# Performance work log

Hardware: AMD Instinct MI355X
Metric: run time of the kernel (lower is better)

The kernel has to match this reference:

```python
import jax, jax.numpy as jnp
import numpy as np

N = 100000   # nodes per node type ('net' and 'cell')
E = 600000   # edges per canonical relation
D_IN = 16    # raw input feature dim
D = 128      # hidden dim (in_size == out_size, required by wl: Linear(2*D -> D))
SLOPE = 0.2  # DGL GATConv leaky_relu negative slope


def setup_inputs() -> dict:
    key = jax.random.key(0)
    ks = jax.random.split(key, 24)
    f = lambda k, shp, scale=1.0: jax.random.normal(k, shp, dtype=jnp.float32) * scale
    s_in = 1.0 / np.sqrt(D_IN).astype(np.float32)
    s_d = 1.0 / np.sqrt(D).astype(np.float32)
    s_2d = 1.0 / np.sqrt(2 * D).astype(np.float32)
    inp = {
        'x_net':   f(ks[0], (N, D_IN)),
        'x_cell':  f(ks[1], (N, D_IN)),
        'Wp_net':  f(ks[2], (D, D_IN), s_in),
        'Wp_cell': f(ks[3], (D, D_IN), s_in),
        # per-edge-type GATConv params: fc weight + attn_l + attn_r (num_heads=1, no bias)
        'Wg0': f(ks[4], (D, D), s_d), 'al0': f(ks[5], (D,), s_d), 'ar0': f(ks[6], (D,), s_d),
        'Wg1': f(ks[7], (D, D), s_d), 'al1': f(ks[8], (D,), s_d), 'ar1': f(ks[9], (D,), s_d),
        'Wg2': f(ks[10], (D, D), s_d), 'al2': f(ks[11], (D,), s_d), 'ar2': f(ks[12], (D,), s_d),
        'Wl':   f(ks[13], (D, 2 * D), s_2d),
        'bias': jnp.zeros((D,), jnp.float32),
        # edge lists: relation 0 = cell->net, 1 = net->cell, 2 = net->net
        'src0': jax.random.randint(ks[14], (E,), 0, N, dtype=jnp.int32),
        'dst0': jax.random.randint(ks[15], (E,), 0, N, dtype=jnp.int32),
        'src1': jax.random.randint(ks[16], (E,), 0, N, dtype=jnp.int32),
        'dst1': jax.random.randint(ks[17], (E,), 0, N, dtype=jnp.int32),
        'src2': jax.random.randint(ks[18], (E,), 0, N, dtype=jnp.int32),
        'dst2': jax.random.randint(ks[19], (E,), 0, N, dtype=jnp.int32),
    }
    return inp


def _gat(x_src, x_dst, W, al, ar, src, dst):
    """DGL GATConv (num_heads=1, bias=False) on one relation's edge list."""
    h_src = x_src @ W.T                               # [N, D]
    h_dst = x_dst @ W.T                               # [N, D]
    el = (h_src @ al)[src]                            # [E] gathered src logits
    er = (h_dst @ ar)[dst]                            # [E] gathered dst logits
    e = jax.nn.leaky_relu(el + er, SLOPE)             # [E]
    # segment softmax over incoming edges of each dst node
    m = jax.ops.segment_max(e, dst, num_segments=N)
    ex = jnp.exp(e - m[dst])
    denom = jax.ops.segment_sum(ex, dst, num_segments=N)
    alpha = ex / denom[dst]                           # [E]
    return jax.ops.segment_sum(h_src[src] * alpha[:, None], dst, num_segments=N)


def reference(x_net, x_cell, Wp_net, Wp_cell,
              Wg0, al0, ar0, Wg1, al1, ar1, Wg2, al2, ar2,
              Wl, bias,
              src0, dst0, src1, dst1, src2, dst2):
    # feature projection per node type (ParaGraph.feat_proj)
    h_net = x_net @ Wp_net.T                          # [N, D]
    h_cell = x_cell @ Wp_cell.T                       # [N, D]
    feat = {'net': h_net, 'cell': h_cell}
    out = {'net': jnp.zeros((N, D), h_net.dtype), 'cell': jnp.zeros((N, D), h_cell.dtype)}
    # canonical etypes: (srctype, dsttype, gat params, edge list)
    rels = [
        ('cell', 'net', Wg0, al0, ar0, src0, dst0),
        ('net', 'cell', Wg1, al1, ar1, src1, dst1),
        ('net', 'net',  Wg2, al2, ar2, src2, dst2),
    ]
    for st, dt, W, al, ar, src, dst in rels:
        out[dt] = out[dt] + _gat(feat[st], feat[dt], W, al, ar, src, dst)
        # faithful to the original: concat+linear+relu recomputed for EVERY ntype
        # inside the etype loop (the redundant fused-op pattern)
        for nt in ('net', 'cell'):
            out[nt] = jax.nn.relu(
                jnp.concatenate([feat[nt], out[nt] + bias], axis=1) @ Wl.T)
    return jnp.stack([out['net'], out['cell']])      # [2, N, D]
```

## Files before the change

### kernel.cpp

```cpp
#include <hip/hip_runtime.h>
#include <hip/hip_bf16.h>
#include <stdint.h>

#define NN 100000
#define NE 600000
#define SP 136
#define NB 782
#define BCAP 1600
#define CHUNK 4096
#define NCH 147
#define GB 1563
#define AB 6250

typedef unsigned short u16;
typedef unsigned int u32;
typedef __attribute__((ext_vector_type(8))) short short8;
typedef __attribute__((ext_vector_type(8))) __bf16 bf16x8;
typedef __attribute__((ext_vector_type(4))) float floatx4;

__device__ __forceinline__ float b2f(u16 u) {
  union { float f; u32 i; } c; c.i = ((u32)u) << 16; return c.f;
}
__device__ __forceinline__ u16 f2b(float f) {
  union { float f; u32 i; } c; c.f = f;
  u32 r = c.i + 0x7FFFu + ((c.i >> 16) & 1u);
  return (u16)(r >> 16);
}


__device__ __forceinline__ void gemm_w(const u16* __restrict__ W, int ldw, u16* __restrict__ C,
                                       u16* lds, int tid, int row0, const bf16x8* a,
                                       int m16, int quad, int wv) {
#pragma unroll
  for (int it = 0; it < 8; ++it) {
    int idx = it * 256 + tid;
    int r = idx >> 4, c = (idx & 15) << 3;
    *(short8*)(&lds[r * SP + c]) = *(const short8*)(W + (size_t)r * ldw + c);
  }
  __syncthreads();
  const u16* brow = &lds[m16 * SP + quad * 8];
  floatx4 acc[8];
#pragma unroll
  for (int c = 0; c < 8; ++c) acc[c] = floatx4{0.f, 0.f, 0.f, 0.f};
#pragma unroll
  for (int kk = 0; kk < 4; ++kk) {
#pragma unroll
    for (int c = 0; c < 8; ++c) {
      bf16x8 bfr = *(const bf16x8*)(brow + c * 16 * SP + kk * 32);
      acc[c] = __builtin_amdgcn_mfma_f32_16x16x32_bf16(a[kk], bfr, acc[c], 0, 0, 0);
    }
  }
#pragma unroll
  for (int c = 0; c < 8; ++c) {
    int col = c * 16 + m16;
#pragma unroll
    for (int r = 0; r < 4; ++r) {
      int grow = row0 + wv * 16 + quad * 4 + r;
      if (grow < NN) C[(size_t)grow * 128 + col] = f2b(acc[c][r]);
    }
  }
}

template<int FINAL>
__device__ __forceinline__ void fused_body(int blk, int tid, const u16* __restrict__ A,
                                           const u16* __restrict__ P, void* __restrict__ C,
                                           const u16* __restrict__ W, const float* __restrict__ cvec,
                                           u16* Wlds) {
  const int row0 = blk * 64;
#pragma unroll
  for (int it = 0; it < 8; ++it) {
    int idx = it * 256 + tid;
    int r = idx >> 4, c = (idx & 15) << 3;
    *(short8*)(&Wlds[r * SP + c]) = *(const short8*)(W + (size_t)r * 256 + c);
  }
  const int lane = tid & 63, wv = tid >> 6;
  const int m16 = lane & 15, quad = lane >> 4;
  int arow = row0 + wv * 16 + m16;
  if (arow >= NN) arow = NN - 1;
  const u16* Ab = A + (size_t)arow * 128 + quad * 8;
  bf16x8 a[4];
#pragma unroll
  for (int kk = 0; kk < 4; ++kk) a[kk] = *(const bf16x8*)(Ab + kk * 32);
  __syncthreads();
  const u16* brow = &Wlds[m16 * SP + quad * 8];
  floatx4 acc[8];
#pragma unroll
  for (int c = 0; c < 8; ++c) acc[c] = floatx4{0.f, 0.f, 0.f, 0.f};
#pragma unroll
  for (int kk = 0; kk < 4; ++kk) {
#pragma unroll
    for (int c = 0; c < 8; ++c) {
      bf16x8 bfr = *(const bf16x8*)(brow + c * 16 * SP + kk * 32);
      acc[c] = __builtin_amdgcn_mfma_f32_16x16x32_bf16(a[kk], bfr, acc[c], 0, 0, 0);
    }
  }
#pragma unroll
  for (int c = 0; c < 8; ++c) {
    int col = c * 16 + m16;
    float cv = cvec[col];
#pragma unroll
    for (int r = 0; r < 4; ++r) {
      int grow = row0 + wv * 16 + quad * 4 + r;
      if (grow < NN) {
        float v = acc[c][r] + b2f(P[(size_t)grow * 128 + col]) + cv;
        v = fmaxf(v, 0.f);
        if (FINAL) ((float*)C)[(size_t)grow * 128 + col] = v;
        else       ((u16*)C)[(size_t)grow * 128 + col] = f2b(v);
      }
    }
  }
}

template<int RMW>
__device__ __forceinline__ void agg_body(int nb, int tid, const u16* __restrict__ h,
                                         const u32* __restrict__ srecs, const int* __restrict__ rp,
                                         const float* __restrict__ el, const float* __restrict__ er,
                                         u16* __restrict__ out) {
  int sub = tid & 15;
  int n = nb * 16 + (tid >> 4);
  int start = rp[n], end = rp[n + 1];
  u16* orow = out + (size_t)n * 128 + sub * 8;
  if (start == end) {
    if (!RMW) *(short8*)orow = short8{0, 0, 0, 0, 0, 0, 0, 0};
    return;
  }
  float ern = er[n];
  float acc[8];
#pragma unroll
  for (int t = 0; t < 8; ++t) acc[t] = 0.f;
  float sl = 0.f;
  const u16* hsub = h + sub * 8;
  for (int base = start; base < end; base += 16) {
    int m = end - base; if (m > 16) m = 16;
    int srci = 0; float w = 0.f;
    if (sub < m) {
      srci = (int)srecs[base + sub];
      float l = el[srci] + ern;
      l = (l >= 0.f) ? l : 0.2f * l;
      w = __expf(l);
    }
    sl += w;
    for (int i = 0; i < m; ++i) {
      float x = __shfl(w, i, 16);
      int sv = __shfl(srci, i, 16);
      short8 hv = *(const short8*)(hsub + (size_t)sv * 128);
#pragma unroll
      for (int t = 0; t < 8; ++t) acc[t] += x * b2f((u16)hv[t]);
    }
  }
  float s = sl;
#pragma unroll
  for (int off = 8; off > 0; off >>= 1) s += __shfl_xor(s, off, 16);
  float inv = 1.f / s;
  short8 o;
  if (RMW) {
    short8 pv = *(const short8*)orow;
#pragma unroll
    for (int t = 0; t < 8; ++t) o[t] = (short)f2b(b2f((u16)pv[t]) + acc[t] * inv);
  } else {
#pragma unroll
    for (int t = 0; t < 8; ++t) o[t] = (short)f2b(acc[t] * inv);
  }
  *(short8*)orow = o;
}


__global__ __launch_bounds__(256) void prep_k(const float* __restrict__ x_net, const float* __restrict__ x_cell,
                                              const float* __restrict__ Wp_net, const float* __restrict__ Wp_cell,
                                              u16* __restrict__ feat_net, u16* __restrict__ feat_cell,
                                              const float* __restrict__ Wl, const float* __restrict__ Wg0,
                                              const float* __restrict__ Wg1, const float* __restrict__ Wg2,
                                              u16* __restrict__ Wl_bf, u16* __restrict__ Wg_bf,
                                              const float* al0, const float* ar0, const float* al1,
                                              const float* ar1, const float* al2, const float* ar2,
                                              const float* bias, float* __restrict__ vecs,
                                              int* __restrict__ bcnt) {
  int bid = blockIdx.x, tid = threadIdx.x;
  if (bid < 2 * AB) {
    int y = bid >= AB;
    int bx = y ? bid - AB : bid;
    const float* x  = y ? x_cell : x_net;
    const float* Wp = y ? Wp_cell : Wp_net;
    u16* feat       = y ? feat_cell : feat_net;
    __shared__ float Ws[128 * 17];
    __shared__ float xs[16][17];
#pragma unroll
    for (int it = 0; it < 8; ++it) {
      int idx = it * 256 + tid;
      int j = idx >> 4, k = idx & 15;
      Ws[j * 17 + k] = Wp[idx];
    }
    int n0 = bx * 16;
    { int nn = tid >> 4, k = tid & 15;
      xs[nn][k] = x[(size_t)(n0 + nn) * 16 + k]; }
    __syncthreads();
    int j = tid & 127, g = tid >> 7;
    float acc[8];
#pragma unroll
    for (int r = 0; r < 8; ++r) acc[r] = 0.f;
#pragma unroll
    for (int k = 0; k < 16; ++k) {
      float w = Ws[j * 17 + k];
#pragma unroll
      for (int r = 0; r < 8; ++r) acc[r] += xs[g * 8 + r][k] * w;
    }
#pragma unroll
    for (int r = 0; r < 8; ++r)
      feat[(size_t)(n0 + g * 8 + r) * 128 + j] = f2b(acc[r]);
  } else if (bid < 2 * AB + 128) {
    int cid = bid - 2 * AB;
    int y = cid >> 5, bx = cid & 31;
    const float* src = (y == 0) ? Wl : (y == 1) ? Wg0 : (y == 2) ? Wg1 : Wg2;
    u16* dst = (y == 0) ? Wl_bf : Wg_bf + (size_t)(y - 1) * 16384;
    int n = (y == 0) ? 32768 : 16384;
    int i = (bx * 256 + tid) * 4;
    if (i >= n) return;
    float4 v = *(const float4*)(src + i);
    ushort4 p; p.x = f2b(v.x); p.y = f2b(v.y); p.z = f2b(v.z); p.w = f2b(v.w);
    *(ushort4*)(dst + i) = p;
  } else if (bid < 2 * AB + 135) {
    int a = bid - (2 * AB + 128);
    if (tid >= 128) return;
    int j = tid;
    float s = 0.f;
    if (a < 6) {
      const float* W = (a < 2) ? Wg0 : (a < 4) ? Wg1 : Wg2;
      const float* v = (a == 0) ? al0 : (a == 1) ? ar0 : (a == 2) ? al1 : (a == 3) ? ar1 : (a == 4) ? al2 : ar2;
      for (int i = 0; i < 128; ++i) s += W[i * 128 + j] * v[i];
    } else {
      for (int i = 0; i < 128; ++i) s += Wl[(size_t)j * 256 + 128 + i] * bias[i];
    }
    vecs[a * 128 + j] = s;
  } else {
    int r = bid - (2 * AB + 135);
    for (int i = tid; i < NB; i += 256) bcnt[(size_t)r * NB + i] = 0;
  }
}

__global__ __launch_bounds__(256) void logbh_k(const u16* __restrict__ feat_net, const u16* __restrict__ feat_cell,
                                               const float* __restrict__ vecs, float* __restrict__ outs,
                                               const int* __restrict__ dst0, const int* __restrict__ dst1,
                                               const int* __restrict__ dst2, int* __restrict__ bcnt) {
  __shared__ int sm[NB];
  int bid = blockIdx.x, tid = threadIdx.x;
  if (bid < 782) {
    float* vs = (float*)sm;
#pragma unroll
    for (int it = 0; it < 3; ++it) vs[it * 256 + tid] = vecs[it * 256 + tid];
    __syncthreads();
    int y = bid >= 391;
    int bx = y ? bid - 391 : bid;
    const u16* f = y ? feat_cell : feat_net;
    int n = bx * 256 + tid;
    if (n >= NN) return;
    const u16* row = f + (size_t)n * 128;
    if (y == 0) {
      float s1 = 0.f, s2 = 0.f, s4 = 0.f, s5 = 0.f;
#pragma unroll
      for (int k = 0; k < 128; k += 8) {
        short8 u = *(const short8*)(row + k);
#pragma unroll
        for (int t = 0; t < 8; ++t) {
          float fv = b2f((u16)u[t]);
          s1 += fv * vs[1 * 128 + k + t]; s2 += fv * vs[2 * 128 + k + t];
          s4 += fv * vs[4 * 128 + k + t]; s5 += fv * vs[5 * 128 + k + t];
        }
      }
      outs[(size_t)1 * NN + n] = s1; outs[(size_t)2 * NN + n] = s2;
      outs[(size_t)4 * NN + n] = s4; outs[(size_t)5 * NN + n] = s5;
    } else {
      float s0 = 0.f, s3 = 0.f;
#pragma unroll
      for (int k = 0; k < 128; k += 8) {
        short8 u = *(const short8*)(row + k);
#pragma unroll
        for (int t = 0; t < 8; ++t) {
          float fv = b2f((u16)u[t]);
          s0 += fv * vs[0 * 128 + k + t]; s3 += fv * vs[3 * 128 + k + t];
        }
      }
      outs[(size_t)0 * NN + n] = s0; outs[(size_t)3 * NN + n] = s3;
    }
  } else {
    int e = bid - 782;
    int r = e / NCH, bx = e % NCH;
    const int* dst = (r == 0) ? dst0 : (r == 1) ? dst1 : dst2;
    for (int i = tid; i < NB; i += 256) sm[i] = 0;
    __syncthreads();
    int e0 = bx * CHUNK;
    int cnt = NE - e0; if (cnt > CHUNK) cnt = CHUNK;
    for (int i = tid; i < cnt; i += 256) atomicAdd(&sm[((u32)dst[e0 + i]) >> 7], 1);
    __syncthreads();
    for (int b = tid; b < NB; b += 256) {
      int c = sm[b];
      if (c) atomicAdd(&bcnt[(size_t)r * NB + b], c);
    }
  }
}

__global__ __launch_bounds__(1024) void bscan_k(const int* __restrict__ bcnt, int* __restrict__ bptr,
                                                int* __restrict__ bcur) {
  int r = blockIdx.x, t = threadIdx.x;
  const int* c = bcnt + (size_t)r * NB;
  int* p = bptr + (size_t)r * (NB + 1);
  int* cur = bcur + (size_t)r * NB;
  int v = (t < NB) ? c[t] : 0;
  __shared__ int ss[1024];
  ss[t] = v; __syncthreads();
  for (int off = 1; off < 1024; off <<= 1) {
    int u = (t >= off) ? ss[t - off] : 0;
    __syncthreads();
    ss[t] += u;
    __syncthreads();
  }
  if (t < NB) { int e = ss[t] - v; p[t] = e; cur[t] = e; }
  if (t == 1023) p[NB] = ss[1023];
}

__global__ __launch_bounds__(256) void bscatter_k(const int* __restrict__ src0, const int* __restrict__ dst0,
                                                  const int* __restrict__ src1, const int* __restrict__ dst1,
                                                  const int* __restrict__ src2, const int* __restrict__ dst2,
                                                  int* __restrict__ bcur, u32* __restrict__ recs) {
  int r = blockIdx.y;
  const int* src = (r == 0) ? src0 : (r == 1) ? src1 : src2;
  const int* dst = (r == 0) ? dst0 : (r == 1) ? dst1 : dst2;
  __shared__ int hist[NB];
  __shared__ int lstart[NB];
  __shared__ int lcur[NB];
  __shared__ int badj[NB];
  __shared__ u32 rbuf[CHUNK];
  __shared__ u16 kbuf[CHUNK];
  __shared__ int ss[256];
  int tid = threadIdx.x;
  int e0 = blockIdx.x * CHUNK;
  int cnt = NE - e0; if (cnt > CHUNK) cnt = CHUNK;

  for (int i = tid; i < NB; i += 256) hist[i] = 0;
  __syncthreads();
  for (int i = tid; i < cnt; i += 256) atomicAdd(&hist[((u32)dst[e0 + i]) >> 7], 1);
  __syncthreads();
  int loc[4]; int s = 0;
  int base4 = tid * 4;
#pragma unroll
  for (int j = 0; j < 4; ++j) {
    int idx = base4 + j;
    int v = (idx < NB) ? hist[idx] : 0;
    loc[j] = s; s += v;
  }
  ss[tid] = s; __syncthreads();
  for (int off = 1; off < 256; off <<= 1) {
    int u = (tid >= off) ? ss[tid - off] : 0;
    __syncthreads();
    ss[tid] += u;
    __syncthreads();
  }
  int ex = ss[tid] - s;
#pragma unroll
  for (int j = 0; j < 4; ++j) {
    int idx = base4 + j;
    if (idx < NB) { int e = ex + loc[j]; lstart[idx] = e; lcur[idx] = e; }
  }
  __syncthreads();
  for (int b = tid; b < NB; b += 256) {
    int c = hist[b];
    int g = 0;
    if (c) g = atomicAdd(&bcur[(size_t)r * NB + b], c);
    badj[b] = g - lstart[b];
  }
  __syncthreads();
  for (int i = tid; i < cnt; i += 256) {
    int dN = dst[e0 + i], sN = src[e0 + i];
    int b = ((u32)dN) >> 7;
    int pos = atomicAdd(&lcur[b], 1);
    rbuf[pos] = ((u32)(dN & 127) << 17) | (u32)sN;
    kbuf[pos] = (u16)b;
  }
  __syncthreads();
  u32* out = recs + (size_t)r * NE;
  for (int i = tid; i < cnt; i += 256) {
    int b = kbuf[i];
    out[badj[b] + i] = rbuf[i];
  }
}

__global__ __launch_bounds__(256) void sortgemm_k(u32* __restrict__ recs, const int* __restrict__ bptr,
                                                  int* __restrict__ rowptr,
                                                  const u16* __restrict__ feat_net, const u16* __restrict__ feat_cell,
                                                  const u16* __restrict__ Wl_bf, const u16* __restrict__ Wg_bf,
                                                  u16* __restrict__ P_net, u16* __restrict__ P_cell,
                                                  u16* __restrict__ h0, u16* __restrict__ h1, u16* __restrict__ h2) {
  __shared__ u32 smem[128 * SP / 2];
  int bid = blockIdx.x, tid = threadIdx.x;
  if (bid < 3 * NB) {
    int r = bid / NB, b = bid % NB;
    const int* p = bptr + (size_t)r * (NB + 1);
    u32* rec = recs + (size_t)r * NE;
    int* rp = rowptr + (size_t)r * (NN + 1);
    int base = p[b], end = p[b + 1];
    int cnt = end - base; if (cnt > BCAP) cnt = BCAP;
    u32* rs = smem;
    int* hist = (int*)(smem + BCAP);
    int* excl = hist + 128;
    int* cur  = excl + 128;
    for (int i = tid; i < cnt; i += 256) rs[i] = rec[base + i];
    if (tid < 128) hist[tid] = 0;
    __syncthreads();
    for (int i = tid; i < cnt; i += 256) atomicAdd(&hist[rs[i] >> 17], 1);
    __syncthreads();
    if (tid < 128) cur[tid] = hist[tid];
    __syncthreads();
    for (int off = 1; off < 128; off <<= 1) {
      int v = 0;
      if (tid < 128 && tid >= off) v = cur[tid - off];
      __syncthreads();
      if (tid < 128) cur[tid] += v;
      __syncthreads();
    }
    if (tid < 128) {
      int e = cur[tid] - hist[tid];
      excl[tid] = e;
      int node = b * 128 + tid;
      if (node < NN) rp[node] = base + e;
    }
    if (b == NB - 1 && tid == 0) rp[NN] = p[NB];
    if (tid < 128) cur[tid] = excl[tid];
    __syncthreads();
    for (int i = tid; i < cnt; i += 256) {
      u32 v = rs[i];
      int pos = atomicAdd(&cur[v >> 17], 1);
      rec[base + pos] = v & 0x1FFFFu;
    }
  } else {
    int g = bid - 3 * NB;
    int ntype = g >= GB;
    int blk = ntype ? g - GB : g;
    u16* lds = (u16*)smem;
    const u16* A = ntype ? feat_cell : feat_net;
    const int row0 = blk * 64;
    const int lane = tid & 63, wv = tid >> 6;
    const int m16 = lane & 15, quad = lane >> 4;
    int arow = row0 + wv * 16 + m16;
    if (arow >= NN) arow = NN - 1;
    const u16* Ab = A + (size_t)arow * 128 + quad * 8;
    bf16x8 a[4];
#pragma unroll
    for (int kk = 0; kk < 4; ++kk) a[kk] = *(const bf16x8*)(Ab + kk * 32);
    if (!ntype) {
      gemm_w(Wl_bf,          256, P_net, lds, tid, row0, a, m16, quad, wv);
      __syncthreads();
      gemm_w(Wg_bf + 16384,  128, h1,    lds, tid, row0, a, m16, quad, wv);
      __syncthreads();
      gemm_w(Wg_bf + 32768,  128, h2,    lds, tid, row0, a, m16, quad, wv);
    } else {
      gemm_w(Wl_bf,          256, P_cell, lds, tid, row0, a, m16, quad, wv);
      __syncthreads();
      gemm_w(Wg_bf,          128, h0,     lds, tid, row0, a, m16, quad, wv);
    }
  }
}

__global__ __launch_bounds__(256) void aggelem_k(const u16* __restrict__ h0, const u32* __restrict__ srecs,
                                                 const int* __restrict__ rp,
                                                 const float* __restrict__ el, const float* __restrict__ er,
                                                 u16* __restrict__ buf_net,
                                                 const u16* __restrict__ P_cell, const float* __restrict__ vecs,
                                                 u16* __restrict__ buf_cell) {
  int bid = blockIdx.x, tid = threadIdx.x;
  if (bid < AB) {
    agg_body<0>(bid, tid, h0, srecs, rp, el, er, buf_net);
  } else {
    __shared__ float cs[128];
    int bx = bid - AB;
    if (tid < 128) cs[tid] = vecs[6 * 128 + tid];
    __syncthreads();
    size_t idx = ((size_t)bx * 256 + tid) * 8;
    if (idx >= (size_t)NN * 128) return;
    int col = (int)(idx & 127);
    short8 u = *(const short8*)(P_cell + idx);
    short8 w;
#pragma unroll
    for (int t = 0; t < 8; ++t)
      w[t] = (short)f2b(fmaxf(b2f((u16)u[t]) + cs[col + t], 0.f));
    *(short8*)(buf_cell + idx) = w;
  }
}

__global__ __launch_bounds__(256) void fusedagg_k(const u16* __restrict__ h1, const u32* __restrict__ srecs,
                                                  const int* __restrict__ rp,
                                                  const float* __restrict__ el, const float* __restrict__ er,
                                                  u16* __restrict__ buf_cell,
                                                  const u16* __restrict__ A, const u16* __restrict__ P_net,
                                                  u16* __restrict__ Cnet,
                                                  const u16* __restrict__ W, const float* __restrict__ cvec) {
  __shared__ u16 Wlds[128 * SP];
  int bid = blockIdx.x, tid = threadIdx.x;
  if (bid < AB) agg_body<1>(bid, tid, h1, srecs, rp, el, er, buf_cell);
  else fused_body<0>(bid - AB, tid, A, P_net, (void*)Cnet, W, cvec, Wlds);
}

__global__ __launch_bounds__(256) void aggfused_k(const u16* __restrict__ h2, const u32* __restrict__ srecs,
                                                  const int* __restrict__ rp,
                                                  const float* __restrict__ el, const float* __restrict__ er,
                                                  u16* __restrict__ buf_net,
                                                  const u16* __restrict__ Acell, const u16* __restrict__ P_cell,
                                                  float* __restrict__ Ccell,
                                                  const u16* __restrict__ W, const float* __restrict__ cvec) {
  __shared__ u16 Wlds[128 * SP];
  int bid = blockIdx.x, tid = threadIdx.x;
  if (bid < AB) agg_body<1>(bid, tid, h2, srecs, rp, el, er, buf_net);
  else fused_body<1>(bid - AB, tid, Acell, P_cell, (void*)Ccell, W, cvec, Wlds);
}

struct FJob { const u16* A; const u16* P; void* C; };
struct FJobs2 { FJob j[2]; const u16* W; const float* cvec; };
template<int FINAL>
__global__ __launch_bounds__(256) void fused_k(FJobs2 jobs) {
  __shared__ u16 Wlds[128 * SP];
  FJob jb = jobs.j[blockIdx.y];
  fused_body<FINAL>(blockIdx.x, threadIdx.x, jb.A, jb.P, jb.C, jobs.W, jobs.cvec, Wlds);
}

extern "C" void kernel_launch(void* const* d_in, const int* in_sizes, int n_in,
                              void* d_out, int out_size, void* d_ws, size_t ws_size,
                              hipStream_t stream) {
  const float* x_net   = (const float*)d_in[0];
  const float* x_cell  = (const float*)d_in[1];
  const float* Wp_net  = (const float*)d_in[2];
  const float* Wp_cell = (const float*)d_in[3];
  const float* Wg[3] = {(const float*)d_in[4], (const float*)d_in[7], (const float*)d_in[10]};
  const float* al[3] = {(const float*)d_in[5], (const float*)d_in[8], (const float*)d_in[11]};
  const float* ar[3] = {(const float*)d_in[6], (const float*)d_in[9], (const float*)d_in[12]};
  const float* Wl    = (const float*)d_in[13];
  const float* bias  = (const float*)d_in[14];
  const int* src[3] = {(const int*)d_in[15], (const int*)d_in[17], (const int*)d_in[19]};
  const int* dst[3] = {(const int*)d_in[16], (const int*)d_in[18], (const int*)d_in[20]};

  char* ws = (char*)d_ws;
  size_t off = 0;
  auto alloc = [&](size_t b) { void* p = ws + off; off = (off + b + 255) & ~(size_t)255; return p; };
  u16*  feat_net  = (u16*)alloc((size_t)NN * 128 * 2);
  u16*  feat_cell = (u16*)alloc((size_t)NN * 128 * 2);
  u16*  hbuf0     = (u16*)alloc((size_t)NN * 128 * 2);
  u16*  hbuf1     = (u16*)alloc((size_t)NN * 128 * 2);
  u16*  hbuf2     = (u16*)alloc((size_t)NN * 128 * 2);
  u16*  P_net     = (u16*)alloc((size_t)NN * 128 * 2);
  u16*  P_cell    = (u16*)alloc((size_t)NN * 128 * 2);
  u16*  buf_net   = (u16*)alloc((size_t)NN * 128 * 2);
  u16*  buf_cell  = (u16*)alloc((size_t)NN * 128 * 2);
  float* vecs     = (float*)alloc(7 * 128 * 4);
  float* logit    = (float*)alloc((size_t)6 * NN * 4);
  u16*   Wl_bf    = (u16*)alloc((size_t)128 * 256 * 2);
  u16*   Wg_bf    = (u16*)alloc((size_t)3 * 128 * 128 * 2);
  int*   bcnt     = (int*)alloc((size_t)3 * NB * 4);
  int*   bcur     = (int*)alloc((size_t)3 * NB * 4);
  int*   bptr     = (int*)alloc((size_t)3 * (NB + 1) * 4);
  int*   rowptr   = (int*)alloc((size_t)3 * (NN + 1) * 4);
  u32*   recs     = (u32*)alloc((size_t)3 * NE * 4);

  float* out_f = (float*)d_out;

  prep_k<<<2 * AB + 138, 256, 0, stream>>>(x_net, x_cell, Wp_net, Wp_cell, feat_net, feat_cell,
                                           Wl, Wg[0], Wg[1], Wg[2], Wl_bf, Wg_bf,
                                           al[0], ar[0], al[1], ar[1], al[2], ar[2], bias, vecs, bcnt);
  logbh_k<<<782 + 3 * NCH, 256, 0, stream>>>(feat_net, feat_cell, vecs, logit,
                                             dst[0], dst[1], dst[2], bcnt);
  bscan_k<<<3, 1024, 0, stream>>>(bcnt, bptr, bcur);
  bscatter_k<<<dim3(NCH, 3), 256, 0, stream>>>(src[0], dst[0], src[1], dst[1], src[2], dst[2],
                                               bcur, recs);
  sortgemm_k<<<3 * NB + 2 * GB, 256, 0, stream>>>(recs, bptr, rowptr, feat_net, feat_cell,
                                                  Wl_bf, Wg_bf, P_net, P_cell, hbuf0, hbuf1, hbuf2);
  aggelem_k<<<2 * AB, 256, 0, stream>>>(hbuf0, recs, rowptr, logit, logit + (size_t)NN, buf_net,
                                        P_cell, vecs, buf_cell);
  fusedagg_k<<<AB + GB, 256, 0, stream>>>(hbuf1, recs + (size_t)NE, rowptr + (NN + 1),
                                          logit + (size_t)2 * NN, logit + (size_t)3 * NN, buf_cell,
                                          buf_net, P_net, buf_net, Wl_bf + 128, vecs + 6 * 128);
  {
    FJobs2 jobs; jobs.W = Wl_bf + 128; jobs.cvec = vecs + 6 * 128;
    jobs.j[0] = {buf_net, P_net, buf_net};
    jobs.j[1] = {buf_cell, P_cell, buf_cell};
    fused_k<0><<<dim3(GB, 2), 256, 0, stream>>>(jobs);
  }
  aggfused_k<<<AB + GB, 256, 0, stream>>>(hbuf2, recs + (size_t)2 * NE, rowptr + 2 * (NN + 1),
                                          logit + (size_t)4 * NN, logit + (size_t)5 * NN, buf_net,
                                          buf_cell, P_cell, out_f + (size_t)NN * 128,
                                          Wl_bf + 128, vecs + 6 * 128);
  {
    FJobs2 jobs; jobs.W = Wl_bf + 128; jobs.cvec = vecs + 6 * 128;
    jobs.j[0] = {buf_net, P_net, out_f};
    jobs.j[1] = jobs.j[0];
    fused_k<1><<<dim3(GB, 1), 256, 0, stream>>>(jobs);
  }
}
```

Baseline: 503.5 us.

## Fuse the post-aggregation concat-linear-relu GEMM into each aggregation block

```diff
diff --git a/kernel.cpp b/kernel.cpp
--- a/kernel.cpp
+++ b/kernel.cpp
@@ -111,57 +111,105 @@
   }
 }
 
-template<int RMW>
-__device__ __forceinline__ void agg_body(int nb, int tid, const u16* __restrict__ h,
-                                         const u32* __restrict__ srecs, const int* __restrict__ rp,
-                                         const float* __restrict__ el, const float* __restrict__ er,
-                                         u16* __restrict__ out) {
+template<int RMW, int FINAL>
+__device__ __forceinline__ void aggF_body(int nb, int tid,
+                                          const u16* __restrict__ h, const u32* __restrict__ srecs,
+                                          const int* __restrict__ rp,
+                                          const float* __restrict__ el, const float* __restrict__ er,
+                                          const u16* __restrict__ prevbuf,
+                                          const u16* __restrict__ P, const float* __restrict__ cvec,
+                                          const u16* __restrict__ W,
+                                          void* __restrict__ out,
+                                          u16* Wlds, u16* Alds) {
+#pragma unroll
+  for (int it = 0; it < 8; ++it) {
+    int idx = it * 256 + tid;
+    int r = idx >> 4, c = (idx & 15) << 3;
+    *(short8*)(&Wlds[r * SP + c]) = *(const short8*)(W + (size_t)r * 256 + c);
+  }
   int sub = tid & 15;
-  int n = nb * 16 + (tid >> 4);
+  int g = tid >> 4;
+  int n = nb * 16 + g;
   int start = rp[n], end = rp[n + 1];
-  u16* orow = out + (size_t)n * 128 + sub * 8;
-  if (start == end) {
-    if (!RMW) *(short8*)orow = short8{0, 0, 0, 0, 0, 0, 0, 0};
-    return;
-  }
-  float ern = er[n];
-  float acc[8];
-#pragma unroll
-  for (int t = 0; t < 8; ++t) acc[t] = 0.f;
-  float sl = 0.f;
-  const u16* hsub = h + sub * 8;
-  for (int base = start; base < end; base += 16) {
-    int m = end - base; if (m > 16) m = 16;
-    int srci = 0; float w = 0.f;
-    if (sub < m) {
-      srci = (int)srecs[base + sub];
-      float l = el[srci] + ern;
-      l = (l >= 0.f) ? l : 0.2f * l;
-      w = __expf(l);
-    }
-    sl += w;
-    for (int i = 0; i < m; ++i) {
-      float x = __shfl(w, i, 16);
-      int sv = __shfl(srci, i, 16);
-      short8 hv = *(const short8*)(hsub + (size_t)sv * 128);
-#pragma unroll
-      for (int t = 0; t < 8; ++t) acc[t] += x * b2f((u16)hv[t]);
-    }
-  }
-  float s = sl;
-#pragma unroll
-  for (int off = 8; off > 0; off >>= 1) s += __shfl_xor(s, off, 16);
-  float inv = 1.f / s;
-  short8 o;
+  float row[8];
   if (RMW) {
-    short8 pv = *(const short8*)orow;
-#pragma unroll
-    for (int t = 0; t < 8; ++t) o[t] = (short)f2b(b2f((u16)pv[t]) + acc[t] * inv);
+    short8 pv = *(const short8*)(prevbuf + (size_t)n * 128 + sub * 8);
+#pragma unroll
+    for (int t = 0; t < 8; ++t) row[t] = b2f((u16)pv[t]);
   } else {
 #pragma unroll
-    for (int t = 0; t < 8; ++t) o[t] = (short)f2b(acc[t] * inv);
-  }
-  *(short8*)orow = o;
+    for (int t = 0; t < 8; ++t) row[t] = 0.f;
+  }
+  if (start < end) {
+    float ern = er[n];
+    float acc[8];
+#pragma unroll
+    for (int t = 0; t < 8; ++t) acc[t] = 0.f;
+    float sl = 0.f;
+    const u16* hsub = h + sub * 8;
+    for (int base = start; base < end; base += 16) {
+      int m = end - base; if (m > 16) m = 16;
+      int srci = 0; float w = 0.f;
+      if (sub < m) {
+        srci = (int)srecs[base + sub];
+        float l = el[srci] + ern;
+        l = (l >= 0.f) ? l : 0.2f * l;
+        w = __expf(l);
+      }
+      sl += w;
+      for (int i = 0; i < m; ++i) {
+        float x = __shfl(w, i, 16);
+        int sv = __shfl(srci, i, 16);
+        short8 hv = *(const short8*)(hsub + (size_t)sv * 128);
+#pragma unroll
+        for (int t = 0; t < 8; ++t) acc[t] += x * b2f((u16)hv[t]);
+      }
+    }
+    float s = sl;
+#pragma unroll
+    for (int off = 8; off > 0; off >>= 1) s += __shfl_xor(s, off, 16);
+    float inv = 1.f / s;
+#pragma unroll
+    for (int t = 0; t < 8; ++t) row[t] += acc[t] * inv;
+  }
+  short8 rb;
+#pragma unroll
+  for (int t = 0; t < 8; ++t) rb[t] = (short)f2b(row[t]);
+  *(short8*)(&Alds[g * SP + sub * 8]) = rb;
+  __syncthreads();
+  const int lane = tid & 63, wv = tid >> 6;
+  const int m16 = lane & 15, quad = lane >> 4;
+  const u16* arow = &Alds[m16 * SP + quad * 8];
+  bf16x8 a[4];
+#pragma unroll
+  for (int kk = 0; kk < 4; ++kk) a[kk] = *(const bf16x8*)(arow + kk * 32);
+  const u16* brow = &Wlds[m16 * SP + quad * 8];
+  floatx4 acc2[2];
+#pragma unroll
+  for (int cc = 0; cc < 2; ++cc) acc2[cc] = floatx4{0.f, 0.f, 0.f, 0.f};
+#pragma unroll
+  for (int kk = 0; kk < 4; ++kk) {
+#pragma unroll
+    for (int cc = 0; cc < 2; ++cc) {
+      int ct = wv * 2 + cc;
+      bf16x8 bfr = *(const bf16x8*)(brow + ct * 16 * SP + kk * 32);
+      acc2[cc] = __builtin_amdgcn_mfma_f32_16x16x32_bf16(a[kk], bfr, acc2[cc], 0, 0, 0);
+    }
+  }
+#pragma unroll
+  for (int cc = 0; cc < 2; ++cc) {
+    int ct = wv * 2 + cc;
+    int col = ct * 16 + m16;
+    float cv = cvec[col];
+#pragma unroll
+    for (int r = 0; r < 4; ++r) {
+      int node = nb * 16 + quad * 4 + r;
+      float v = acc2[cc][r] + b2f(P[(size_t)node * 128 + col]) + cv;
+      v = fmaxf(v, 0.f);
+      if (FINAL) ((float*)out)[(size_t)node * 128 + col] = v;
+      else       ((u16*)out)[(size_t)node * 128 + col] = f2b(v);
+    }
+  }
 }
 
 
@@ -391,8 +439,34 @@
                                                   u16* __restrict__ h0, u16* __restrict__ h1, u16* __restrict__ h2) {
   __shared__ u32 smem[128 * SP / 2];
   int bid = blockIdx.x, tid = threadIdx.x;
-  if (bid < 3 * NB) {
-    int r = bid / NB, b = bid % NB;
+  if (bid < 2 * GB) {
+    int ntype = bid >= GB;
+    int blk = ntype ? bid - GB : bid;
+    u16* lds = (u16*)smem;
+    const u16* A = ntype ? feat_cell : feat_net;
+    const int row0 = blk * 64;
+    const int lane = tid & 63, wv = tid >> 6;
+    const int m16 = lane & 15, quad = lane >> 4;
+    int arow = row0 + wv * 16 + m16;
+    if (arow >= NN) arow = NN - 1;
+    const u16* Ab = A + (size_t)arow * 128 + quad * 8;
+    bf16x8 a[4];
+#pragma unroll
+    for (int kk = 0; kk < 4; ++kk) a[kk] = *(const bf16x8*)(Ab + kk * 32);
+    if (!ntype) {
+      gemm_w(Wl_bf,          256, P_net, lds, tid, row0, a, m16, quad, wv);
+      __syncthreads();
+      gemm_w(Wg_bf + 16384,  128, h1,    lds, tid, row0, a, m16, quad, wv);
+      __syncthreads();
+      gemm_w(Wg_bf + 32768,  128, h2,    lds, tid, row0, a, m16, quad, wv);
+    } else {
+      gemm_w(Wl_bf,          256, P_cell, lds, tid, row0, a, m16, quad, wv);
+      __syncthreads();
+      gemm_w(Wg_bf,          128, h0,     lds, tid, row0, a, m16, quad, wv);
+    }
+  } else {
+    int sb = bid - 2 * GB;
+    int r = sb / NB, b = sb % NB;
     const int* p = bptr + (size_t)r * (NB + 1);
     u32* rec = recs + (size_t)r * NE;
     int* rp = rowptr + (size_t)r * (NN + 1);
@@ -430,48 +504,25 @@
       int pos = atomicAdd(&cur[v >> 17], 1);
       rec[base + pos] = v & 0x1FFFFu;
     }
-  } else {
-    int g = bid - 3 * NB;
-    int ntype = g >= GB;
-    int blk = ntype ? g - GB : g;
-    u16* lds = (u16*)smem;
-    const u16* A = ntype ? feat_cell : feat_net;
-    const int row0 = blk * 64;
-    const int lane = tid & 63, wv = tid >> 6;
-    const int m16 = lane & 15, quad = lane >> 4;
-    int arow = row0 + wv * 16 + m16;
-    if (arow >= NN) arow = NN - 1;
-    const u16* Ab = A + (size_t)arow * 128 + quad * 8;
-    bf16x8 a[4];
-#pragma unroll
-    for (int kk = 0; kk < 4; ++kk) a[kk] = *(const bf16x8*)(Ab + kk * 32);
-    if (!ntype) {
-      gemm_w(Wl_bf,          256, P_net, lds, tid, row0, a, m16, quad, wv);
-      __syncthreads();
-      gemm_w(Wg_bf + 16384,  128, h1,    lds, tid, row0, a, m16, quad, wv);
-      __syncthreads();
-      gemm_w(Wg_bf + 32768,  128, h2,    lds, tid, row0, a, m16, quad, wv);
-    } else {
-      gemm_w(Wl_bf,          256, P_cell, lds, tid, row0, a, m16, quad, wv);
-      __syncthreads();
-      gemm_w(Wg_bf,          128, h0,     lds, tid, row0, a, m16, quad, wv);
-    }
   }
 }
 
 __global__ __launch_bounds__(256) void aggelem_k(const u16* __restrict__ h0, const u32* __restrict__ srecs,
                                                  const int* __restrict__ rp,
                                                  const float* __restrict__ el, const float* __restrict__ er,
-                                                 u16* __restrict__ buf_net,
-                                                 const u16* __restrict__ P_cell, const float* __restrict__ vecs,
-                                                 u16* __restrict__ buf_cell) {
+                                                 const u16* __restrict__ P_net, const float* __restrict__ cvec,
+                                                 const u16* __restrict__ W2, u16* __restrict__ buf_net,
+                                                 const u16* __restrict__ P_cell, u16* __restrict__ buf_cell) {
+  __shared__ u16 Wlds[128 * SP];
+  __shared__ u16 Alds[16 * SP];
   int bid = blockIdx.x, tid = threadIdx.x;
   if (bid < AB) {
-    agg_body<0>(bid, tid, h0, srecs, rp, el, er, buf_net);
+    aggF_body<0, 0>(bid, tid, h0, srecs, rp, el, er, nullptr, P_net, cvec, W2,
+                    (void*)buf_net, Wlds, Alds);
   } else {
-    __shared__ float cs[128];
+    float* cs = (float*)Alds;
     int bx = bid - AB;
-    if (tid < 128) cs[tid] = vecs[6 * 128 + tid];
+    if (tid < 128) cs[tid] = cvec[tid];
     __syncthreads();
     size_t idx = ((size_t)bx * 256 + tid) * 8;
     if (idx >= (size_t)NN * 128) return;
@@ -485,39 +536,41 @@
   }
 }
 
-__global__ __launch_bounds__(256) void fusedagg_k(const u16* __restrict__ h1, const u32* __restrict__ srecs,
-                                                  const int* __restrict__ rp,
-                                                  const float* __restrict__ el, const float* __restrict__ er,
-                                                  u16* __restrict__ buf_cell,
-                                                  const u16* __restrict__ A, const u16* __restrict__ P_net,
-                                                  u16* __restrict__ Cnet,
-                                                  const u16* __restrict__ W, const float* __restrict__ cvec) {
+__global__ __launch_bounds__(256) void aggfused1_k(const u16* __restrict__ h1, const u32* __restrict__ srecs,
+                                                   const int* __restrict__ rp,
+                                                   const float* __restrict__ el, const float* __restrict__ er,
+                                                   const u16* __restrict__ P_cell, u16* __restrict__ buf_cell,
+                                                   const u16* __restrict__ buf_net, const u16* __restrict__ P_net,
+                                                   u16* __restrict__ buf_net_out,
+                                                   const u16* __restrict__ W2, const float* __restrict__ cvec) {
   __shared__ u16 Wlds[128 * SP];
+  __shared__ u16 Alds[16 * SP];
   int bid = blockIdx.x, tid = threadIdx.x;
-  if (bid < AB) agg_body<1>(bid, tid, h1, srecs, rp, el, er, buf_cell);
-  else fused_body<0>(bid - AB, tid, A, P_net, (void*)Cnet, W, cvec, Wlds);
-}
-
-__global__ __launch_bounds__(256) void aggfused_k(const u16* __restrict__ h2, const u32* __restrict__ srecs,
-                                                  const int* __restrict__ rp,
-                                                  const float* __restrict__ el, const float* __restrict__ er,
-                                                  u16* __restrict__ buf_net,
-                                                  const u16* __restrict__ Acell, const u16* __restrict__ P_cell,
-                                                  float* __restrict__ Ccell,
-                                                  const u16* __restrict__ W, const float* __restrict__ cvec) {
+  if (bid < AB) {
+    aggF_body<1, 0>(bid, tid, h1, srecs, rp, el, er, buf_cell, P_cell, cvec, W2,
+                    (void*)buf_cell, Wlds, Alds);
+  } else {
+    fused_body<0>(bid - AB, tid, buf_net, P_net, (void*)buf_net_out, W2, cvec, Wlds);
+  }
+}
+
+__global__ __launch_bounds__(256) void aggfused2_k(const u16* __restrict__ h2, const u32* __restrict__ srecs,
+                                                   const int* __restrict__ rp,
+                                                   const float* __restrict__ el, const float* __restrict__ er,
+                                                   const u16* __restrict__ buf_net, const u16* __restrict__ P_net,
+                                                   float* __restrict__ out_net,
+                                                   const u16* __restrict__ buf_cell, const u16* __restrict__ P_cell,
+                                                   float* __restrict__ out_cell,
+                                                   const u16* __restrict__ W2, const float* __restrict__ cvec) {
   __shared__ u16 Wlds[128 * SP];
+  __shared__ u16 Alds[16 * SP];
   int bid = blockIdx.x, tid = threadIdx.x;
-  if (bid < AB) agg_body<1>(bid, tid, h2, srecs, rp, el, er, buf_net);
-  else fused_body<1>(bid - AB, tid, Acell, P_cell, (void*)Ccell, W, cvec, Wlds);
-}
-
-struct FJob { const u16* A; const u16* P; void* C; };
-struct FJobs2 { FJob j[2]; const u16* W; const float* cvec; };
-template<int FINAL>
-__global__ __launch_bounds__(256) void fused_k(FJobs2 jobs) {
-  __shared__ u16 Wlds[128 * SP];
-  FJob jb = jobs.j[blockIdx.y];
-  fused_body<FINAL>(blockIdx.x, threadIdx.x, jb.A, jb.P, jb.C, jobs.W, jobs.cvec, Wlds);
+  if (bid < AB) {
+    aggF_body<1, 1>(bid, tid, h2, srecs, rp, el, er, buf_net, P_net, cvec, W2,
+                    (void*)out_net, Wlds, Alds);
+  } else {
+    fused_body<1>(bid - AB, tid, buf_cell, P_cell, (void*)out_cell, W2, cvec, Wlds);
+  }
 }
 
 extern "C" void kernel_launch(void* const* d_in, const int* in_sizes, int n_in,
@@ -558,6 +611,8 @@
   u32*   recs     = (u32*)alloc((size_t)3 * NE * 4);
 
   float* out_f = (float*)d_out;
+  const u16* W2 = Wl_bf + 128;
+  const float* cvec = vecs + 6 * 128;
 
   prep_k<<<2 * AB + 138, 256, 0, stream>>>(x_net, x_cell, Wp_net, Wp_cell, feat_net, feat_cell,
                                            Wl, Wg[0], Wg[1], Wg[2], Wl_bf, Wg_bf,
@@ -567,27 +622,15 @@
   bscan_k<<<3, 1024, 0, stream>>>(bcnt, bptr, bcur);
   bscatter_k<<<dim3(NCH, 3), 256, 0, stream>>>(src[0], dst[0], src[1], dst[1], src[2], dst[2],
                                                bcur, recs);
-  sortgemm_k<<<3 * NB + 2 * GB, 256, 0, stream>>>(recs, bptr, rowptr, feat_net, feat_cell,
+  sortgemm_k<<<2 * GB + 3 * NB, 256, 0, stream>>>(recs, bptr, rowptr, feat_net, feat_cell,
                                                   Wl_bf, Wg_bf, P_net, P_cell, hbuf0, hbuf1, hbuf2);
-  aggelem_k<<<2 * AB, 256, 0, stream>>>(hbuf0, recs, rowptr, logit, logit + (size_t)NN, buf_net,
-                                        P_cell, vecs, buf_cell);
-  fusedagg_k<<<AB + GB, 256, 0, stream>>>(hbuf1, recs + (size_t)NE, rowptr + (NN + 1),
-                                          logit + (size_t)2 * NN, logit + (size_t)3 * NN, buf_cell,
-                                          buf_net, P_net, buf_net, Wl_bf + 128, vecs + 6 * 128);
-  {
-    FJobs2 jobs; jobs.W = Wl_bf + 128; jobs.cvec = vecs + 6 * 128;
-    jobs.j[0] = {buf_net, P_net, buf_net};
-    jobs.j[1] = {buf_cell, P_cell, buf_cell};
-    fused_k<0><<<dim3(GB, 2), 256, 0, stream>>>(jobs);
-  }
-  aggfused_k<<<AB + GB, 256, 0, stream>>>(hbuf2, recs + (size_t)2 * NE, rowptr + 2 * (NN + 1),
-                                          logit + (size_t)4 * NN, logit + (size_t)5 * NN, buf_net,
-                                          buf_cell, P_cell, out_f + (size_t)NN * 128,
-                                          Wl_bf + 128, vecs + 6 * 128);
-  {
-    FJobs2 jobs; jobs.W = Wl_bf + 128; jobs.cvec = vecs + 6 * 128;
-    jobs.j[0] = {buf_net, P_net, out_f};
-    jobs.j[1] = jobs.j[0];
-    fused_k<1><<<dim3(GB, 1), 256, 0, stream>>>(jobs);
-  }
-}
+  aggelem_k<<<2 * AB, 256, 0, stream>>>(hbuf0, recs, rowptr, logit, logit + (size_t)NN,
+                                        P_net, cvec, W2, buf_net, P_cell, buf_cell);
+  aggfused1_k<<<AB + GB, 256, 0, stream>>>(hbuf1, recs + (size_t)NE, rowptr + (NN + 1),
+                                           logit + (size_t)2 * NN, logit + (size_t)3 * NN,
+                                           P_cell, buf_cell, buf_net, P_net, buf_net, W2, cvec);
+  aggfused2_k<<<AB + GB, 256, 0, stream>>>(hbuf2, recs + (size_t)2 * NE, rowptr + 2 * (NN + 1),
+                                           logit + (size_t)4 * NN, logit + (size_t)5 * NN,
+                                           buf_net, P_net, out_f,
+                                           buf_cell, P_cell, out_f + (size_t)NN * 128, W2, cvec);
+}
```

New measurement: 469.9 us. 1.07x faster.
